# Kernel tuning notes

Measured on AMD Instinct MI355X. Metric: run time of the kernel, lower is better.

The kernel has to match this reference:

```python
import jax, jax.numpy as jnp
import numpy as np

B, T, N_AGENTS = 256, 200, 8
OBS_DIM, OUT_DIM, RNN_IN, RNN_H = 128, 16, 64, 64
IN_DIM = OBS_DIM + N_AGENTS  # 136


def setup_inputs() -> dict:
    key = jax.random.key(0)
    ks = jax.random.split(key, 8)
    def lin(k, fan_out, fan_in):
        bound = 1.0 / np.sqrt(fan_in)
        return jax.random.uniform(k, (fan_out, fan_in), jnp.float32, -bound, bound)
    obs_history = jax.random.normal(ks[0], (B, T, N_AGENTS, OBS_DIM), jnp.float32)
    # agent id per slot n, constant over batch/time (ids 0..N_AGENTS-1)
    agent = jnp.broadcast_to(jnp.arange(N_AGENTS, dtype=jnp.int32)[None, None, :, None],
                             (B, T, N_AGENTS, 1))
    return {
        "obs_history": obs_history,
        "agent": agent,
        "W1": lin(ks[1], RNN_IN, IN_DIM),
        "b1": jnp.zeros((RNN_IN,), jnp.float32),
        "W_ih": lin(ks[2], 3 * RNN_H, RNN_IN),
        "W_hh": lin(ks[3], 3 * RNN_H, RNN_H),
        "b_ih": jnp.zeros((3 * RNN_H,), jnp.float32),
        "b_hh": jnp.zeros((3 * RNN_H,), jnp.float32),
        "W2": lin(ks[4], OUT_DIM, RNN_H),
        "b2": jnp.zeros((OUT_DIM,), jnp.float32),
    }


def _drqn_scan(x, W1, b1, W_ih, W_hh, b_ih, b_hh, W2, b2):
    # x: [T, BN, IN_DIM]
    def step(h, xt):
        a = jax.nn.relu(xt @ W1.T + b1)                 # fc1: [BN, RNN_IN]
        gi = a @ W_ih.T + b_ih                          # [BN, 3H]
        gh = h @ W_hh.T + b_hh                          # [BN, 3H]
        i_r, i_z, i_n = jnp.split(gi, 3, axis=-1)
        h_r, h_z, h_n = jnp.split(gh, 3, axis=-1)
        r = jax.nn.sigmoid(i_r + h_r)
        z = jax.nn.sigmoid(i_z + h_z)
        n = jnp.tanh(i_n + r * h_n)
        h_new = (1.0 - z) * n + z * h                   # GRUCell update
        q = h_new @ W2.T + b2                           # fc2: [BN, OUT]
        return h_new, q
    h0 = jnp.zeros((x.shape[1], RNN_H), x.dtype)
    _, qs = jax.lax.scan(step, h0, x)
    return qs  # [T, BN, OUT]


def reference(obs_history, agent, W1, b1, W_ih, W_hh, b_ih, b_hh, W2, b2):
    # agent id per slot n (constant over batch/time): agent[0,...,n,:].max()
    agent_ids = jnp.max(agent[0, :, :, 0], axis=0)                 # [N]
    oh = jax.nn.one_hot(agent_ids, N_AGENTS, dtype=obs_history.dtype)  # [N, N_AGENTS]
    oh_b = jnp.broadcast_to(oh[None, None], (B, T, N_AGENTS, N_AGENTS))
    x = jnp.concatenate([obs_history, oh_b], axis=-1)              # [B,T,N,IN]
    x = jnp.transpose(x, (1, 0, 2, 3)).reshape(T, B * N_AGENTS, IN_DIM)
    qs = _drqn_scan(x, W1, b1, W_ih, W_hh, b_ih, b_hh, W2, b2)     # [T,BN,OUT]
    nn_output = jnp.transpose(qs.reshape(T, B, N_AGENTS, OUT_DIM), (1, 0, 2, 3))
    # per-agent max over that agent's valid action dim (all = OUT_DIM here)
    action_dims = [OUT_DIM] * N_AGENTS
    max_values = jnp.stack(
        [jnp.max(nn_output[..., n, :action_dims[n]], axis=-1) for n in range(N_AGENTS)], axis=-1)
    max_actions = jnp.stack(
        [jnp.argmax(nn_output[..., n, :action_dims[n]], axis=-1) for n in range(N_AGENTS)],
        axis=-1).astype(jnp.float32)
    return nn_output, max_values, max_actions
```

## Files before the change

kernel.cpp:

```cpp
#include <hip/hip_runtime.h>


namespace {
constexpr int kB = 256, kT = 200, kN = 8, kObs = 128, kH = 64, kOut = 16;
constexpr int kRows = kB * kT * kN;
constexpr size_t kABytes  = (size_t)kRows * 64 * 4;
constexpr size_t kGiBytes = (size_t)kRows * 192 * 4;
}

__global__ __launch_bounds__(256, 2)
void fc1_k(const float* __restrict__ obs, const int* __restrict__ agent,
           const float* __restrict__ W1, const float* __restrict__ b1,
           float* __restrict__ a_out) {
  __shared__ float xs[2][2][128];
  __shared__ float ps[2][2][64];
  __shared__ float ohs[512];
  const int tid = threadIdx.x, lane = tid & 63, w = tid >> 6;
  const int e = w >> 1, p = w & 1;

  for (int i = tid; i < 512; i += 256) {
    int n = i >> 6, l = i & 63;
    ohs[i] = W1[(size_t)l * 136 + 128 + agent[n]];
  }

  float4 wv[16];
  #pragma unroll
  for (int k = 0; k < 16; ++k)
    wv[k] = *(const float4*)(W1 + (size_t)lane * 136 + p * 64 + k * 4);
  const float b1r = b1[lane];

  constexpr int ROWS = 100;
  const int eng = blockIdx.x * 2 + e;
  const int r0 = eng * ROWS;
  const int et = p * 64 + lane;

  xs[e][0][et] = obs[(size_t)r0 * 128 + et];
  float xq = obs[(size_t)(r0 + 1) * 128 + et];
  __syncthreads();

  #pragma unroll 1
  for (int i = 0; i < ROWS; ++i) {
    const int r = r0 + i;
    if (i + 1 < ROWS) xs[e][(i + 1) & 1][et] = xq;
    const int nr = (i + 2 < ROWS) ? (r0 + i + 2) : (r0 + ROWS - 1);
    xq = obs[(size_t)nr * 128 + et];

    const float* xb = xs[e][i & 1] + p * 64;
    float a0 = 0.f, a1 = 0.f, a2 = 0.f, a3 = 0.f;
    #pragma unroll
    for (int k = 0; k < 16; ++k) {
      float4 xp = *(const float4*)(xb + k * 4);
      a0 = fmaf(wv[k].x, xp.x, a0);
      a1 = fmaf(wv[k].y, xp.y, a1);
      a2 = fmaf(wv[k].z, xp.z, a2);
      a3 = fmaf(wv[k].w, xp.w, a3);
    }
    const float part = (a0 + a1) + (a2 + a3);
    if (p == 0) ps[e][i & 1][lane] = part;
    __syncthreads();
    if (p == 1) {
      float av = part + ps[e][i & 1][lane] + b1r + ohs[(r & 7) * 64 + lane];
      a_out[(size_t)r * 64 + lane] = fmaxf(av, 0.f);
    }
  }
}

__global__ __launch_bounds__(256, 2)
void gi_k(const float* __restrict__ a_glob, const float* __restrict__ Wih,
          const float* __restrict__ bih, float* __restrict__ gi_out) {
  __shared__ float as_[4][2][64];
  const int tid = threadIdx.x, lane = tid & 63, w = tid >> 6;

  float wir[64], wiz[64], win_[64];
  #pragma unroll
  for (int k = 0; k < 64; k += 4) {
    *(float4*)&wir[k]  = *(const float4*)(Wih + (size_t)lane * 64 + k);
    *(float4*)&wiz[k]  = *(const float4*)(Wih + (size_t)(64 + lane) * 64 + k);
    *(float4*)&win_[k] = *(const float4*)(Wih + (size_t)(128 + lane) * 64 + k);
  }
  const float bir = bih[lane], biz = bih[64 + lane], bin_ = bih[128 + lane];

  const int gwave = blockIdx.x * 4 + w;
  const int r0 = gwave * 200;
  float (*ab)[64] = as_[w];

  ab[0][lane] = a_glob[(size_t)r0 * 64 + lane];
  float qA = a_glob[(size_t)(r0 + 1) * 64 + lane];
  float qB = a_glob[(size_t)(r0 + 2) * 64 + lane];

#define GI_BODY(T, Q, NEXT)                                                    \
  {                                                                            \
    const int t_ = (T);                                                        \
    if (t_ < 199) ab[(t_ + 1) & 1][lane] = Q;                                  \
    const int nr_ = (NEXT) > 199 ? 199 : (NEXT);                               \
    Q = a_glob[(size_t)(r0 + nr_) * 64 + lane];                                \
    const float* ap_ = ab[t_ & 1];                                             \
    float r0a = bir, r1a = 0.f, z0a = biz, z1a = 0.f, n0a = bin_, n1a = 0.f;   \
    _Pragma("unroll") for (int k = 0; k < 64; k += 4) {                        \
      float4 av = *(const float4*)(ap_ + k);                                   \
      r0a = fmaf(wir[k], av.x, r0a);  r1a = fmaf(wir[k + 1], av.y, r1a);       \
      r0a = fmaf(wir[k + 2], av.z, r0a); r1a = fmaf(wir[k + 3], av.w, r1a);    \
      z0a = fmaf(wiz[k], av.x, z0a);  z1a = fmaf(wiz[k + 1], av.y, z1a);       \
      z0a = fmaf(wiz[k + 2], av.z, z0a); z1a = fmaf(wiz[k + 3], av.w, z1a);    \
      n0a = fmaf(win_[k], av.x, n0a); n1a = fmaf(win_[k + 1], av.y, n1a);      \
      n0a = fmaf(win_[k + 2], av.z, n0a); n1a = fmaf(win_[k + 3], av.w, n1a);  \
    }                                                                          \
    float* gp_ = gi_out + (size_t)(r0 + t_) * 192;                             \
    gp_[lane] = r0a + r1a;                                                     \
    gp_[64 + lane] = z0a + z1a;                                                \
    gp_[128 + lane] = n0a + n1a;                                               \
  }

  #pragma unroll 1
  for (int i = 0; i < 200; i += 2) {
    GI_BODY(i + 0, qA, i + 3)
    GI_BODY(i + 1, qB, i + 4)
  }
#undef GI_BODY
}

__global__ __launch_bounds__(256, 2)
void gru3_k(const float* __restrict__ gi_glob,
            const float* __restrict__ Whh, const float* __restrict__ bhh,
            const float* __restrict__ W2, const float* __restrict__ b2,
            float* __restrict__ out) {
  __shared__ float hs[4][64];
  const int tid = threadIdx.x, lane = tid & 63, w = tid >> 6;
  float* hsw = hs[w];

  float whr[64], whz[64], whn[64];
  #pragma unroll
  for (int k = 0; k < 64; k += 4) {
    *(float4*)&whr[k] = *(const float4*)(Whh + (size_t)lane * 64 + k);
    *(float4*)&whz[k] = *(const float4*)(Whh + (size_t)(64 + lane) * 64 + k);
    *(float4*)&whn[k] = *(const float4*)(Whh + (size_t)(128 + lane) * 64 + k);
  }
  const float bhr = bhh[lane], bhz = bhh[64 + lane], bhn = bhh[128 + lane];
  const int m = lane & 15, qt = lane >> 4;
  float w2r[16];
  #pragma unroll
  for (int j = 0; j < 16; j += 4)
    *(float4*)&w2r[j] = *(const float4*)(W2 + (size_t)m * 64 + qt * 16 + j);
  const float b2r = b2[m];

  const int s = blockIdx.x * 4 + w;
  const int b = s >> 3, n = s & 7;
  const size_t rbase = (size_t)b * 1600 + n;

  float* outq  = out;
  float* outmv = out + (size_t)kRows * 16;
  float* outma = outmv + kRows;

  hsw[lane] = 0.f;
  float h = 0.f;

  const float* gp0 = gi_glob + rbase * 192;
  float gA0 = gp0[lane], gA1 = gp0[64 + lane], gA2 = gp0[128 + lane];
  const float* gp1 = gi_glob + (rbase + 8) * 192;
  float gB0 = gp1[lane], gB1 = gp1[64 + lane], gB2 = gp1[128 + lane];

#define GRU_STEP(T, G0, G1, G2, TN)                                            \
  {                                                                            \
    const int t_ = (T);                                                        \
    const size_t r_ = rbase + (size_t)t_ * 8;                                  \
    float hr0 = bhr, hr1 = 0.f, hz0 = bhz, hz1 = 0.f, hn0 = bhn, hn1 = 0.f;    \
    _Pragma("unroll") for (int k = 0; k < 64; k += 4) {                        \
      float4 hp = *(const float4*)(hsw + k);                                   \
      hr0 = fmaf(whr[k], hp.x, hr0);  hr1 = fmaf(whr[k + 1], hp.y, hr1);       \
      hr0 = fmaf(whr[k + 2], hp.z, hr0); hr1 = fmaf(whr[k + 3], hp.w, hr1);    \
      hz0 = fmaf(whz[k], hp.x, hz0);  hz1 = fmaf(whz[k + 1], hp.y, hz1);       \
      hz0 = fmaf(whz[k + 2], hp.z, hz0); hz1 = fmaf(whz[k + 3], hp.w, hz1);    \
      hn0 = fmaf(whn[k], hp.x, hn0);  hn1 = fmaf(whn[k + 1], hp.y, hn1);       \
      hn0 = fmaf(whn[k + 2], hp.z, hn0); hn1 = fmaf(whn[k + 3], hp.w, hn1);    \
    }                                                                          \
    const float rg = 1.f / (1.f + __expf(-((G0) + hr0 + hr1)));                \
    const float zg = 1.f / (1.f + __expf(-((G1) + hz0 + hz1)));                \
    const float e2 = __expf(2.f * ((G2) + rg * (hn0 + hn1)));                  \
    const float ng = 1.f - 2.f / (e2 + 1.f);                                   \
    h = (1.f - zg) * ng + zg * h;                                              \
    hsw[lane] = h;                                                             \
    const int tn_ = (TN) > 199 ? 199 : (TN);                                   \
    const float* gp_ = gi_glob + (rbase + (size_t)tn_ * 8) * 192;              \
    G0 = gp_[lane]; G1 = gp_[64 + lane]; G2 = gp_[128 + lane];                 \
    float q0 = 0.f, q1 = 0.f;                                                  \
    _Pragma("unroll") for (int j = 0; j < 16; j += 4) {                        \
      float4 hp = *(const float4*)(hsw + qt * 16 + j);                         \
      q0 = fmaf(w2r[j], hp.x, q0);     q1 = fmaf(w2r[j + 1], hp.y, q1);        \
      q0 = fmaf(w2r[j + 2], hp.z, q0); q1 = fmaf(w2r[j + 3], hp.w, q1);        \
    }                                                                          \
    float q = q0 + q1;                                                         \
    q += __shfl_xor(q, 16);                                                    \
    q += __shfl_xor(q, 32);                                                    \
    q += b2r;                                                                  \
    if (lane < 16) outq[r_ * 16 + m] = q;                                      \
    float bv = q; int bi = m;                                                  \
    _Pragma("unroll") for (int d = 1; d < 16; d <<= 1) {                       \
      float ov = __shfl_xor(bv, d, 16);                                        \
      int oi = __shfl_xor(bi, d, 16);                                          \
      if (ov > bv || (ov == bv && oi < bi)) { bv = ov; bi = oi; }              \
    }                                                                          \
    if (lane == 0) { outmv[r_] = bv; outma[r_] = (float)bi; }                  \
  }

  #pragma unroll 1
  for (int t = 0; t < 200; t += 2) {
    GRU_STEP(t, gA0, gA1, gA2, t + 2)
    GRU_STEP(t + 1, gB0, gB1, gB2, t + 3)
  }
#undef GRU_STEP
}

namespace fb {
constexpr int kW1Pitch = 137, kHPitch = 65;
constexpr int OFF_W1 = 0;
constexpr int OFF_WIH = OFF_W1 + 64 * kW1Pitch;
constexpr int OFF_WHH = OFF_WIH + 192 * kHPitch;
constexpr int OFF_W2 = OFF_WHH + 192 * kHPitch;
constexpr int OFF_B1 = OFF_W2 + 16 * kHPitch;
constexpr int OFF_BIH = OFF_B1 + 64;
constexpr int OFF_BHH = OFF_BIH + 192;
constexpr int OFF_B2 = OFF_BHH + 192;
constexpr int LDS_FLOATS = OFF_B2 + 16;
}

__device__ __forceinline__ float bcastf(float v, int l) {
  return __int_as_float(__builtin_amdgcn_readlane(__float_as_int(v), l));
}

__global__ __launch_bounds__(512, 1)
void drqn_fused(const float* __restrict__ obs, const int* __restrict__ agent,
                const float* __restrict__ W1, const float* __restrict__ b1,
                const float* __restrict__ Wih, const float* __restrict__ Whh,
                const float* __restrict__ bih, const float* __restrict__ bhh,
                const float* __restrict__ W2, const float* __restrict__ b2,
                float* __restrict__ out) {
  using namespace fb;
  extern __shared__ float lds[];
  float* W1s = lds + OFF_W1; float* Wihs = lds + OFF_WIH;
  float* Whhs = lds + OFF_WHH; float* W2s = lds + OFF_W2;
  float* b1s = lds + OFF_B1; float* bihs = lds + OFF_BIH;
  float* bhhs = lds + OFF_BHH; float* b2s = lds + OFF_B2;
  const int tid = threadIdx.x;
  for (int i = tid; i < 64 * 136; i += 512) { int r = i / 136, c = i - r * 136; W1s[r * kW1Pitch + c] = W1[i]; }
  for (int i = tid; i < 192 * 64; i += 512) { int r = i >> 6, c = i & 63; Wihs[r * kHPitch + c] = Wih[i]; }
  for (int i = tid; i < 192 * 64; i += 512) { int r = i >> 6, c = i & 63; Whhs[r * kHPitch + c] = Whh[i]; }
  for (int i = tid; i < 16 * 64; i += 512) { int r = i >> 6, c = i & 63; W2s[r * kHPitch + c] = W2[i]; }
  if (tid < 64) b1s[tid] = b1[tid];
  if (tid < 192) bihs[tid] = bih[tid];
  if (tid < 192) bhhs[tid] = bhh[tid];
  if (tid < 16) b2s[tid] = b2[tid];
  __syncthreads();
  const int wave = tid >> 6, lane = tid & 63;
  const int s = blockIdx.x * 8 + wave;
  const int b = s >> 3, n = s & 7;
  const int acol = 128 + agent[n];
  const float* obase = obs + (((size_t)b * kT) * kN + n) * kObs;
  const size_t qbase = (((size_t)b * kT) * kN + n) * kOut;
  const size_t mbase = ((size_t)b * kT) * kN + n;
  float* outq = out;
  float* outmv = out + (size_t)kB * kT * kN * kOut;
  float* outma = outmv + (size_t)kB * kT * kN;
  float h = 0.f;
  float xa = obase[lane], xb = obase[64 + lane];
  #pragma unroll 1
  for (int t = 0; t < kT; ++t) {
    float xan = 0.f, xbn = 0.f;
    if (t + 1 < kT) { const float* p = obase + (size_t)(t + 1) * kN * kObs; xan = p[lane]; xbn = p[64 + lane]; }
    float acc = b1s[lane] + W1s[lane * kW1Pitch + acol];
    #pragma unroll
    for (int k = 0; k < 64; ++k) acc += W1s[lane * kW1Pitch + k] * bcastf(xa, k);
    #pragma unroll
    for (int k = 0; k < 64; ++k) acc += W1s[lane * kW1Pitch + 64 + k] * bcastf(xb, k);
    float a = fmaxf(acc, 0.f);
    float air = bihs[lane], aiz = bihs[64 + lane], ain = bihs[128 + lane];
    #pragma unroll
    for (int k = 0; k < 64; ++k) {
      float sa = bcastf(a, k);
      air += Wihs[lane * kHPitch + k] * sa;
      aiz += Wihs[(64 + lane) * kHPitch + k] * sa;
      ain += Wihs[(128 + lane) * kHPitch + k] * sa;
    }
    float ghr = bhhs[lane], ghz = bhhs[64 + lane], ghn = bhhs[128 + lane];
    #pragma unroll
    for (int k = 0; k < 64; ++k) {
      float sh = bcastf(h, k);
      ghr += Whhs[lane * kHPitch + k] * sh;
      ghz += Whhs[(64 + lane) * kHPitch + k] * sh;
      ghn += Whhs[(128 + lane) * kHPitch + k] * sh;
    }
    float rg = 1.f / (1.f + expf(-(air + ghr)));
    float zg = 1.f / (1.f + expf(-(aiz + ghz)));
    float ng = tanhf(ain + rg * ghn);
    h = (1.f - zg) * ng + zg * h;
    const int m = lane & 15;
    float q = b2s[m];
    #pragma unroll
    for (int k = 0; k < 64; ++k) q += W2s[m * kHPitch + k] * bcastf(h, k);
    if (lane < 16) outq[qbase + (size_t)t * kN * kOut + m] = q;
    float bv = q; int bi = m;
    #pragma unroll
    for (int d = 1; d < 16; d <<= 1) {
      float ov = __shfl_xor(bv, d, 16);
      int oi = __shfl_xor(bi, d, 16);
      if (ov > bv || (ov == bv && oi < bi)) { bv = ov; bi = oi; }
    }
    if (lane == 0) { outmv[mbase + (size_t)t * kN] = bv; outma[mbase + (size_t)t * kN] = (float)bi; }
    xa = xan; xb = xbn;
  }
}

extern "C" void kernel_launch(void* const* d_in, const int* in_sizes, int n_in,
                              void* d_out, int out_size, void* d_ws, size_t ws_size,
                              hipStream_t stream) {
  const float* obs  = (const float*)d_in[0];
  const int* agent  = (const int*)d_in[1];
  const float* W1   = (const float*)d_in[2];
  const float* b1   = (const float*)d_in[3];
  const float* Wih  = (const float*)d_in[4];
  const float* Whh  = (const float*)d_in[5];
  const float* bih  = (const float*)d_in[6];
  const float* bhh  = (const float*)d_in[7];
  const float* W2   = (const float*)d_in[8];
  const float* b2   = (const float*)d_in[9];
  float* out = (float*)d_out;

  if (ws_size >= kABytes + kGiBytes) {
    float* a_buf  = (float*)d_ws;
    float* gi_buf = (float*)((char*)d_ws + kABytes);
    fc1_k<<<dim3(2048), dim3(256), 0, stream>>>(obs, agent, W1, b1, a_buf);
    gi_k<<<dim3(512), dim3(256), 0, stream>>>(a_buf, Wih, bih, gi_buf);
    gru3_k<<<dim3(512), dim3(256), 0, stream>>>(gi_buf, Whh, bhh, W2, b2, out);
  } else {
    (void)hipFuncSetAttribute((const void*)drqn_fused,
                              hipFuncAttributeMaxDynamicSharedMemorySize,
                              fb::LDS_FLOATS * 4);
    drqn_fused<<<dim3(256), dim3(512), fb::LDS_FLOATS * 4, stream>>>(
        obs, agent, W1, b1, Wih, Whh, bih, bhh, W2, b2, out);
  }
}
```

Measured before the change: 715.2 us.

## Split GRU gates across waves and move fc2/argmax into a separate kernel

The input-gate kernel now assigns one gate per wave, so each wave keeps 64 weight registers instead of 192 and three times as many waves run. The recurrent kernel uses a 192-thread block per sequence, one wave per gate, and exchanges r/z and the hidden state through LDS with two block barriers per step. Hidden states are written into the reused fc1 buffer, and a new fc2q kernel computes Q-values and the max/argmax from them in parallel. This raises occupancy on the serial recurrence, at the cost of per-step barriers, an extra launch and extra global traffic for the hidden states.

New measurement: 888.2 us. 24.2% more time.

```diff
diff --git a/kernel.cpp b/kernel.cpp
--- a/kernel.cpp
+++ b/kernel.cpp
@@ -66,76 +66,115 @@
 }
 
 __global__ __launch_bounds__(256, 2)
-void gi_k(const float* __restrict__ a_glob, const float* __restrict__ Wih,
-          const float* __restrict__ bih, float* __restrict__ gi_out) {
+void gi5_k(const float* __restrict__ a_glob, const float* __restrict__ Wih,
+           const float* __restrict__ bih, float* __restrict__ gi_out) {
   __shared__ float as_[4][2][64];
   const int tid = threadIdx.x, lane = tid & 63, w = tid >> 6;
-
-  float wir[64], wiz[64], win_[64];
+  const int W = blockIdx.x * 4 + w;
+  const int eng = W / 3, g = W - eng * 3;
+
+  float wg[64];
   #pragma unroll
-  for (int k = 0; k < 64; k += 4) {
-    *(float4*)&wir[k]  = *(const float4*)(Wih + (size_t)lane * 64 + k);
-    *(float4*)&wiz[k]  = *(const float4*)(Wih + (size_t)(64 + lane) * 64 + k);
-    *(float4*)&win_[k] = *(const float4*)(Wih + (size_t)(128 + lane) * 64 + k);
-  }
-  const float bir = bih[lane], biz = bih[64 + lane], bin_ = bih[128 + lane];
-
-  const int gwave = blockIdx.x * 4 + w;
-  const int r0 = gwave * 200;
+  for (int k = 0; k < 64; k += 4)
+    *(float4*)&wg[k] = *(const float4*)(Wih + (size_t)(g * 64 + lane) * 64 + k);
+  const float bg = bih[g * 64 + lane];
+
+  const int r0 = eng * 200;
   float (*ab)[64] = as_[w];
-
   ab[0][lane] = a_glob[(size_t)r0 * 64 + lane];
-  float qA = a_glob[(size_t)(r0 + 1) * 64 + lane];
-  float qB = a_glob[(size_t)(r0 + 2) * 64 + lane];
-
-#define GI_BODY(T, Q, NEXT)                                                    \
+  float aq = a_glob[(size_t)(r0 + 1) * 64 + lane];
+
+  #pragma unroll 1
+  for (int i = 0; i < 200; ++i) {
+    const int r = r0 + i;
+    if (i + 1 < 200) ab[(i + 1) & 1][lane] = aq;
+    const int nr = (i + 2 < 200) ? (r0 + i + 2) : (r0 + 199);
+    aq = a_glob[(size_t)nr * 64 + lane];
+
+    const float* ap = ab[i & 1];
+    float a0 = 0.f, a1 = 0.f;
+    #pragma unroll
+    for (int k = 0; k < 64; k += 4) {
+      float4 av = *(const float4*)(ap + k);
+      a0 = fmaf(wg[k],     av.x, a0);
+      a1 = fmaf(wg[k + 1], av.y, a1);
+      a0 = fmaf(wg[k + 2], av.z, a0);
+      a1 = fmaf(wg[k + 3], av.w, a1);
+    }
+    gi_out[(size_t)r * 192 + g * 64 + lane] = bg + a0 + a1;
+  }
+}
+
+__global__ __launch_bounds__(192, 2)
+void gru5_k(const float* __restrict__ gi_glob,
+            const float* __restrict__ Whh, const float* __restrict__ bhh,
+            float* __restrict__ h_out) {
+  __shared__ float hsb[2][64];
+  __shared__ float rgs[64];
+  __shared__ float zgs[64];
+  const int tid = threadIdx.x, lane = tid & 63, g = tid >> 6;
+
+  float wg[64];
+  #pragma unroll
+  for (int k = 0; k < 64; k += 4)
+    *(float4*)&wg[k] = *(const float4*)(Whh + (size_t)(g * 64 + lane) * 64 + k);
+  const float bg = bhh[g * 64 + lane];
+
+  const int s = blockIdx.x;
+  const size_t rbase = (size_t)(s >> 3) * 1600 + (s & 7);
+  const float* gip = gi_glob + rbase * 192 + g * 64 + lane;
+
+  if (g == 0) hsb[0][lane] = 0.f;
+  float h = 0.f;
+  float giA = gip[0];
+  float giB = gip[1536];
+  __syncthreads();
+
+#define GRU5_STEP(T, G, TN)                                                    \
   {                                                                            \
     const int t_ = (T);                                                        \
-    if (t_ < 199) ab[(t_ + 1) & 1][lane] = Q;                                  \
-    const int nr_ = (NEXT) > 199 ? 199 : (NEXT);                               \
-    Q = a_glob[(size_t)(r0 + nr_) * 64 + lane];                                \
-    const float* ap_ = ab[t_ & 1];                                             \
-    float r0a = bir, r1a = 0.f, z0a = biz, z1a = 0.f, n0a = bin_, n1a = 0.f;   \
+    const int cur_ = t_ & 1;                                                   \
+    const float* hb_ = hsb[cur_];                                              \
+    float a0 = 0.f, a1 = 0.f;                                                  \
     _Pragma("unroll") for (int k = 0; k < 64; k += 4) {                        \
-      float4 av = *(const float4*)(ap_ + k);                                   \
-      r0a = fmaf(wir[k], av.x, r0a);  r1a = fmaf(wir[k + 1], av.y, r1a);       \
-      r0a = fmaf(wir[k + 2], av.z, r0a); r1a = fmaf(wir[k + 3], av.w, r1a);    \
-      z0a = fmaf(wiz[k], av.x, z0a);  z1a = fmaf(wiz[k + 1], av.y, z1a);       \
-      z0a = fmaf(wiz[k + 2], av.z, z0a); z1a = fmaf(wiz[k + 3], av.w, z1a);    \
-      n0a = fmaf(win_[k], av.x, n0a); n1a = fmaf(win_[k + 1], av.y, n1a);      \
-      n0a = fmaf(win_[k + 2], av.z, n0a); n1a = fmaf(win_[k + 3], av.w, n1a);  \
+      float4 hp = *(const float4*)(hb_ + k);                                   \
+      a0 = fmaf(wg[k],     hp.x, a0);                                          \
+      a1 = fmaf(wg[k + 1], hp.y, a1);                                          \
+      a0 = fmaf(wg[k + 2], hp.z, a0);                                          \
+      a1 = fmaf(wg[k + 3], hp.w, a1);                                          \
     }                                                                          \
-    float* gp_ = gi_out + (size_t)(r0 + t_) * 192;                             \
-    gp_[lane] = r0a + r1a;                                                     \
-    gp_[64 + lane] = z0a + z1a;                                                \
-    gp_[128 + lane] = n0a + n1a;                                               \
-  }
-
-  #pragma unroll 1
-  for (int i = 0; i < 200; i += 2) {
-    GI_BODY(i + 0, qA, i + 3)
-    GI_BODY(i + 1, qB, i + 4)
-  }
-#undef GI_BODY
+    const float acc_ = bg + a0 + a1;                    \
+    const float gi_ = (G);                                                     \
+    const int tn_ = (TN) > 199 ? 199 : (TN);                                   \
+    (G) = gip[(size_t)tn_ * 1536];                                             \
+    if (g == 0)      rgs[lane] = 1.f / (1.f + __expf(-(gi_ + acc_)));          \
+    else if (g == 1) zgs[lane] = 1.f / (1.f + __expf(-(gi_ + acc_)));          \
+    __syncthreads();                                     \
+    if (g == 2) {                                                              \
+      const float rg_ = rgs[lane], zg_ = zgs[lane];                            \
+      const float e2_ = __expf(2.f * (gi_ + rg_ * acc_));                      \
+      const float ng_ = 1.f - 2.f / (e2_ + 1.f);                     \
+      h = (1.f - zg_) * ng_ + zg_ * h;                                         \
+      hsb[cur_ ^ 1][lane] = h;                                                 \
+      h_out[(rbase + (size_t)t_ * 8) * 64 + lane] = h;                         \
+    }                                                                          \
+    __syncthreads();                                        \
+  }
+
+  #pragma unroll 1
+  for (int t = 0; t < 200; t += 2) {
+    GRU5_STEP(t,     giA, t + 2)
+    GRU5_STEP(t + 1, giB, t + 3)
+  }
+#undef GRU5_STEP
 }
 
 __global__ __launch_bounds__(256, 2)
-void gru3_k(const float* __restrict__ gi_glob,
-            const float* __restrict__ Whh, const float* __restrict__ bhh,
+void fc2q_k(const float* __restrict__ h_all,
             const float* __restrict__ W2, const float* __restrict__ b2,
             float* __restrict__ out) {
-  __shared__ float hs[4][64];
+  __shared__ float hs[4][2][64];
   const int tid = threadIdx.x, lane = tid & 63, w = tid >> 6;
-  float* hsw = hs[w];
-
-  float whr[64], whz[64], whn[64];
-  #pragma unroll
-  for (int k = 0; k < 64; k += 4) {
-    *(float4*)&whr[k] = *(const float4*)(Whh + (size_t)lane * 64 + k);
-    *(float4*)&whz[k] = *(const float4*)(Whh + (size_t)(64 + lane) * 64 + k);
-    *(float4*)&whn[k] = *(const float4*)(Whh + (size_t)(128 + lane) * 64 + k);
-  }
-  const float bhr = bhh[lane], bhz = bhh[64 + lane], bhn = bhh[128 + lane];
   const int m = lane & 15, qt = lane >> 4;
   float w2r[16];
   #pragma unroll
@@ -143,71 +182,50 @@
     *(float4*)&w2r[j] = *(const float4*)(W2 + (size_t)m * 64 + qt * 16 + j);
   const float b2r = b2[m];
 
-  const int s = blockIdx.x * 4 + w;
-  const int b = s >> 3, n = s & 7;
-  const size_t rbase = (size_t)b * 1600 + n;
+  constexpr int ROWS = 100;
+  const int gwave = blockIdx.x * 4 + w;
+  const int r0 = gwave * ROWS;
+  float (*hw)[64] = hs[w];
 
   float* outq  = out;
   float* outmv = out + (size_t)kRows * 16;
   float* outma = outmv + kRows;
 
-  hsw[lane] = 0.f;
-  float h = 0.f;
-
-  const float* gp0 = gi_glob + rbase * 192;
-  float gA0 = gp0[lane], gA1 = gp0[64 + lane], gA2 = gp0[128 + lane];
-  const float* gp1 = gi_glob + (rbase + 8) * 192;
-  float gB0 = gp1[lane], gB1 = gp1[64 + lane], gB2 = gp1[128 + lane];
-
-#define GRU_STEP(T, G0, G1, G2, TN)                                            \
-  {                                                                            \
-    const int t_ = (T);                                                        \
-    const size_t r_ = rbase + (size_t)t_ * 8;                                  \
-    float hr0 = bhr, hr1 = 0.f, hz0 = bhz, hz1 = 0.f, hn0 = bhn, hn1 = 0.f;    \
-    _Pragma("unroll") for (int k = 0; k < 64; k += 4) {                        \
-      float4 hp = *(const float4*)(hsw + k);                                   \
-      hr0 = fmaf(whr[k], hp.x, hr0);  hr1 = fmaf(whr[k + 1], hp.y, hr1);       \
-      hr0 = fmaf(whr[k + 2], hp.z, hr0); hr1 = fmaf(whr[k + 3], hp.w, hr1);    \
-      hz0 = fmaf(whz[k], hp.x, hz0);  hz1 = fmaf(whz[k + 1], hp.y, hz1);       \
-      hz0 = fmaf(whz[k + 2], hp.z, hz0); hz1 = fmaf(whz[k + 3], hp.w, hz1);    \
-      hn0 = fmaf(whn[k], hp.x, hn0);  hn1 = fmaf(whn[k + 1], hp.y, hn1);       \
-      hn0 = fmaf(whn[k + 2], hp.z, hn0); hn1 = fmaf(whn[k + 3], hp.w, hn1);    \
-    }                                                                          \
-    const float rg = 1.f / (1.f + __expf(-((G0) + hr0 + hr1)));                \
-    const float zg = 1.f / (1.f + __expf(-((G1) + hz0 + hz1)));                \
-    const float e2 = __expf(2.f * ((G2) + rg * (hn0 + hn1)));                  \
-    const float ng = 1.f - 2.f / (e2 + 1.f);                                   \
-    h = (1.f - zg) * ng + zg * h;                                              \
-    hsw[lane] = h;                                                             \
-    const int tn_ = (TN) > 199 ? 199 : (TN);                                   \
-    const float* gp_ = gi_glob + (rbase + (size_t)tn_ * 8) * 192;              \
-    G0 = gp_[lane]; G1 = gp_[64 + lane]; G2 = gp_[128 + lane];                 \
-    float q0 = 0.f, q1 = 0.f;                                                  \
-    _Pragma("unroll") for (int j = 0; j < 16; j += 4) {                        \
-      float4 hp = *(const float4*)(hsw + qt * 16 + j);                         \
-      q0 = fmaf(w2r[j], hp.x, q0);     q1 = fmaf(w2r[j + 1], hp.y, q1);        \
-      q0 = fmaf(w2r[j + 2], hp.z, q0); q1 = fmaf(w2r[j + 3], hp.w, q1);        \
-    }                                                                          \
-    float q = q0 + q1;                                                         \
-    q += __shfl_xor(q, 16);                                                    \
-    q += __shfl_xor(q, 32);                                                    \
-    q += b2r;                                                                  \
-    if (lane < 16) outq[r_ * 16 + m] = q;                                      \
-    float bv = q; int bi = m;                                                  \
-    _Pragma("unroll") for (int d = 1; d < 16; d <<= 1) {                       \
-      float ov = __shfl_xor(bv, d, 16);                                        \
-      int oi = __shfl_xor(bi, d, 16);                                          \
-      if (ov > bv || (ov == bv && oi < bi)) { bv = ov; bi = oi; }              \
-    }                                                                          \
-    if (lane == 0) { outmv[r_] = bv; outma[r_] = (float)bi; }                  \
-  }
-
-  #pragma unroll 1
-  for (int t = 0; t < 200; t += 2) {
-    GRU_STEP(t, gA0, gA1, gA2, t + 2)
-    GRU_STEP(t + 1, gB0, gB1, gB2, t + 3)
-  }
-#undef GRU_STEP
+  hw[0][lane] = h_all[(size_t)r0 * 64 + lane];
+  float hq = h_all[(size_t)(r0 + 1) * 64 + lane];
+
+  #pragma unroll 1
+  for (int i = 0; i < ROWS; ++i) {
+    const int r = r0 + i;
+    if (i + 1 < ROWS) hw[(i + 1) & 1][lane] = hq;
+    const int nr = (i + 2 < ROWS) ? (r0 + i + 2) : (r0 + ROWS - 1);
+    hq = h_all[(size_t)nr * 64 + lane];
+
+    const float* hb = hw[i & 1] + qt * 16;
+    float q0 = 0.f, q1 = 0.f;
+    #pragma unroll
+    for (int j = 0; j < 16; j += 4) {
+      float4 hp = *(const float4*)(hb + j);
+      q0 = fmaf(w2r[j],     hp.x, q0);
+      q1 = fmaf(w2r[j + 1], hp.y, q1);
+      q0 = fmaf(w2r[j + 2], hp.z, q0);
+      q1 = fmaf(w2r[j + 3], hp.w, q1);
+    }
+    float q = q0 + q1;
+    q += __shfl_xor(q, 16);
+    q += __shfl_xor(q, 32);
+    q += b2r;
+    if (lane < 16) outq[(size_t)r * 16 + m] = q;
+
+    float bv = q; int bi = m;
+    #pragma unroll
+    for (int d = 1; d < 16; d <<= 1) {
+      float ov = __shfl_xor(bv, d, 16);
+      int oi = __shfl_xor(bi, d, 16);
+      if (ov > bv || (ov == bv && oi < bi)) { bv = ov; bi = oi; }
+    }
+    if (lane == 0) { outmv[r] = bv; outma[r] = (float)bi; }
+  }
 }
 
 namespace fb {
@@ -327,9 +345,10 @@
   if (ws_size >= kABytes + kGiBytes) {
     float* a_buf  = (float*)d_ws;
     float* gi_buf = (float*)((char*)d_ws + kABytes);
-    fc1_k<<<dim3(2048), dim3(256), 0, stream>>>(obs, agent, W1, b1, a_buf);
-    gi_k<<<dim3(512), dim3(256), 0, stream>>>(a_buf, Wih, bih, gi_buf);
-    gru3_k<<<dim3(512), dim3(256), 0, stream>>>(gi_buf, Whh, bhh, W2, b2, out);
+    fc1_k <<<dim3(2048), dim3(256), 0, stream>>>(obs, agent, W1, b1, a_buf);
+    gi5_k <<<dim3(1536), dim3(256), 0, stream>>>(a_buf, Wih, bih, gi_buf);
+    gru5_k<<<dim3(2048), dim3(192), 0, stream>>>(gi_buf, Whh, bhh, a_buf);
+    fc2q_k<<<dim3(1024), dim3(256), 0, stream>>>(a_buf, W2, b2, out);
   } else {
     (void)hipFuncSetAttribute((const void*)drqn_fused,
                               hipFuncAttributeMaxDynamicSharedMemorySize,
```
